# Optimization experiments

Hardware: AMD Instinct MI355X
Metric: run time of the kernel (lower is better)

## Reference

```python
import jax, jax.numpy as jnp
import numpy as np
import math

BLUR, P, SCALING = 0.05, 2.0, 0.9
DIAMETER = 8.0  # static bound on max |x-y| for unit-normal 1-D data (geomloss derives it from data)
NEG = -1e9     # masked log-weight


def _eps_schedule():
    # geomloss epsilon_schedule: diameter^p -> blur^p, geometric with ratio scaling^p
    eps = [DIAMETER ** P]
    eps += list(np.exp(np.arange(P * math.log(DIAMETER), P * math.log(BLUR), P * math.log(SCALING))))
    eps += [BLUR ** P]
    return np.asarray(eps, dtype=np.float32)


def _softmin(eps, C, h):
    # h: [m] = log-weights + dual/eps ; returns [n] = -eps*logsumexp_j(h_j - C_ij/eps)
    return -eps * jax.nn.logsumexp(h[None, :] - C / eps, axis=1)


def _sinkhorn_divergence(x, y, logw):
    # x, y: [B] 1-D point clouds for one output dim; logw: [B] masked log-weights.
    # Debiased Sinkhorn divergence S = OT_eps(a,b) - 0.5 OT(a,a) - 0.5 OT(b,b), p=2 cost |x-y|^2/2.
    Cxy = 0.5 * (x[:, None] - y[None, :]) ** 2
    Cxx = 0.5 * (x[:, None] - x[None, :]) ** 2
    Cyy = 0.5 * (y[:, None] - y[None, :]) ** 2
    eps_list = jnp.asarray(_eps_schedule())
    e0 = eps_list[0]
    f = _softmin(e0, Cxy, logw)    # dual on x for OT(a,b)
    g = _softmin(e0, Cxy.T, logw)  # dual on y for OT(a,b)
    a = _softmin(e0, Cxx, logw)    # self dual on x
    b = _softmin(e0, Cyy, logw)    # self dual on y

    def step(carry, eps):
        f, g, a, b = carry
        ft = _softmin(eps, Cxy, logw + g / eps)
        gt = _softmin(eps, Cxy.T, logw + f / eps)
        at = _softmin(eps, Cxx, logw + a / eps)
        bt = _softmin(eps, Cyy, logw + b / eps)
        return (0.5 * (f + ft), 0.5 * (g + gt), 0.5 * (a + at), 0.5 * (b + bt)), None

    (f, g, a, b), _ = jax.lax.scan(step, (f, g, a, b), eps_list)
    # last extrapolation at final eps (full updates, no damping)
    e = eps_list[-1]
    f, g = _softmin(e, Cxy, logw + g / e), _softmin(e, Cxy.T, logw + f / e)
    a = 0.5 * (a + _softmin(e, Cxx, logw + a / e))
    b = 0.5 * (b + _softmin(e, Cyy, logw + b / e))
    w = jnp.exp(logw)  # 1/n on valid samples, 0 on masked
    return jnp.sum(w * (f - a)) + jnp.sum(w * (g - b))


def reference(predictions, targets):
    # predictions, targets: [B, D]; NaNs in targets mark invalid samples per dim
    mask = ~jnp.isnan(targets)                      # [B, D]
    y = jnp.where(mask, targets, 0.0)
    counts = jnp.sum(mask, axis=0)                  # [D]
    logn = jnp.log(jnp.maximum(counts, 1).astype(predictions.dtype))
    logw = jnp.where(mask, -logn[None, :], NEG)     # [B, D]
    per_dim = jax.vmap(_sinkhorn_divergence, in_axes=(1, 1, 1))(predictions, y, logw)
    per_dim = jnp.where(counts > 1, per_dim, 0.0)   # dims with <=1 valid sample -> 0
    total = jnp.mean(per_dim)                       # weights=None -> mean over dims
    return total, per_dim


def setup_inputs() -> dict:
    key = jax.random.key(0)
    k1, k2, k3 = jax.random.split(key, 3)
    B, D = 2048, 8
    preds = jax.random.normal(k1, (B, D), dtype=jnp.float32)
    targ = jax.random.normal(k2, (B, D), dtype=jnp.float32)
    nan_mask = jax.random.uniform(k3, (B, D)) < 0.1
    targ = jnp.where(nan_mask, jnp.nan, targ)
    return {"predictions": preds, "targets": targ}
```

## Files before the change

kernel.cpp:

```cpp
#include <hip/hip_runtime.h>
#include <math.h>

#define BN 2048
#define DN 8
#define NEGW -1e9f
#define TPB 256
#define RPB 64
#define RS 16
#define JSPLIT 16
#define SLOTS (BN/2)
#define SPC (SLOTS/JSPLIT)
#define CPAD 65

typedef float f2 __attribute__((ext_vector_type(2)));

static __device__ __forceinline__ float wave_reduce_sum(float v){
  #pragma unroll
  for (int off = 32; off > 0; off >>= 1) v += __shfl_xor(v, off, 64);
  return v;
}

__global__ void setup_kernel(const float* __restrict__ pred, const float* __restrict__ targ,
                             float* __restrict__ xcol, float* __restrict__ ycol,
                             float* __restrict__ logw, float* __restrict__ counts){
  int d = blockIdx.x;
  int t = threadIdx.x;
  int lane = t & 63, wave = t >> 6;
  float mk[BN/256];
  float c = 0.f;
  for (int k = 0; k < BN/256; k++){
    int i = t + k*256;
    float tv = targ[i*DN + d];
    bool m = !(tv != tv);
    mk[k] = m ? 1.f : 0.f;
    c += mk[k];
    ycol[d*BN + i] = m ? tv : 0.f;
    xcol[d*BN + i] = pred[i*DN + d];
  }
  __shared__ float sh[4];
  __shared__ float logn_sh;
  float cw = wave_reduce_sum(c);
  if (lane == 0) sh[wave] = cw;
  __syncthreads();
  if (t == 0){
    float tot = sh[0] + sh[1] + sh[2] + sh[3];
    counts[d] = tot;
    logn_sh = logf(fmaxf(tot, 1.f));
  }
  __syncthreads();
  float ln = logn_sh;
  for (int k = 0; k < BN/256; k++){
    int i = t + k*256;
    logw[d*BN + i] = (mk[k] > 0.f) ? -ln : NEGW;
  }
}

__global__ __launch_bounds__(TPB) void sink_step(
      const float* __restrict__ xcol, const float* __restrict__ ycol,
      const float* __restrict__ logw,
      const float* __restrict__ dold, float* __restrict__ dnew,
      float eps, float inv_eps, int mode){
  const float L2E = 1.44269504088896340736f;
  const float LN2 = 0.69314718055994530942f;
  __shared__ float4 pair4[JSPLIT*CPAD];
  __shared__ float pm[JSPLIT][RPB];
  __shared__ float ps[JSPLIT][RPB];
  __shared__ float mmx[RPB];

  int bid = blockIdx.x;
  int rc  = bid & 31;
  int mat = (bid >> 5) & 3;
  int d   = bid >> 7;
  int t   = threadIdx.x;
  int rs  = t & (RS-1);
  int jc  = t >> 4;

  const float* xb = xcol + d*BN;
  const float* yb = ycol + d*BN;
  const float* lw = logw + d*BN;
  const float* ri; const float* pj; int hsel;
  switch (mat){
    case 0:  ri = xb; pj = yb; hsel = 1; break;
    case 1:  ri = yb; pj = xb; hsel = 0; break;
    case 2:  ri = xb; pj = xb; hsel = 2; break;
    default: ri = yb; pj = yb; hsel = 3; break;
  }
  const float* hd  = dold + (size_t)hsel*DN*BN + d*BN;
  const float* dmp = dold + (size_t)mat *DN*BN + d*BN;
  float*       op  = dnew + (size_t)mat *DN*BN + d*BN;

  const float c1 = L2E * inv_eps;
  const float c2 = 0.5f * inv_eps * L2E;

  const float2* pj2 = (const float2*)pj;
  const float2* lw2 = (const float2*)lw;
  const float2* hd2 = (const float2*)hd;
  #pragma unroll
  for (int k = 0; k < SLOTS/TPB; k++){
    int idx = t + k*TPB;
    int phys = idx + (idx >> 6);
    float2 y2 = pj2[idx];
    float2 l2 = lw2[idx];
    float h0 = l2.x, h1 = l2.y;
    if (mode != 0){
      float2 dd = hd2[idx];
      h0 = fmaf(dd.x, inv_eps, h0);
      h1 = fmaf(dd.y, inv_eps, h1);
    }
    pair4[phys] = make_float4(y2.x, y2.y,
                              fmaf(-c2*y2.x, y2.x, L2E*h0),
                              fmaf(-c2*y2.y, y2.y, L2E*h1));
  }

  int row0 = rc*RPB + rs;
  f2 a2[4];
  #pragma unroll
  for (int r = 0; r < 4; r++){
    float xi = ri[row0 + RS*r];
    float al = c1 * xi;
    a2[r] = (f2){al, al};
  }
  __syncthreads();

  const float4* cb = pair4 + jc*CPAD;
  f2 m2[4];
  #pragma unroll
  for (int r = 0; r < 4; r++) m2[r] = (f2){-INFINITY, -INFINITY};
  #pragma unroll 1
  for (int q = 0; q < SPC; q += 8){
    float4 P0 = cb[q+0]; float4 P1 = cb[q+1];
    float4 P2 = cb[q+2]; float4 P3 = cb[q+3];
    float4 P4 = cb[q+4]; float4 P5 = cb[q+5];
    float4 P6 = cb[q+6]; float4 P7 = cb[q+7];
    #pragma unroll
    for (int r = 0; r < 4; r++){
      f2 a = a2[r], mm = m2[r];
      mm = __builtin_elementwise_max(mm, __builtin_elementwise_fma(a, (f2){P0.x,P0.y}, (f2){P0.z,P0.w}));
      mm = __builtin_elementwise_max(mm, __builtin_elementwise_fma(a, (f2){P1.x,P1.y}, (f2){P1.z,P1.w}));
      mm = __builtin_elementwise_max(mm, __builtin_elementwise_fma(a, (f2){P2.x,P2.y}, (f2){P2.z,P2.w}));
      mm = __builtin_elementwise_max(mm, __builtin_elementwise_fma(a, (f2){P3.x,P3.y}, (f2){P3.z,P3.w}));
      mm = __builtin_elementwise_max(mm, __builtin_elementwise_fma(a, (f2){P4.x,P4.y}, (f2){P4.z,P4.w}));
      mm = __builtin_elementwise_max(mm, __builtin_elementwise_fma(a, (f2){P5.x,P5.y}, (f2){P5.z,P5.w}));
      mm = __builtin_elementwise_max(mm, __builtin_elementwise_fma(a, (f2){P6.x,P6.y}, (f2){P6.z,P6.w}));
      mm = __builtin_elementwise_max(mm, __builtin_elementwise_fma(a, (f2){P7.x,P7.y}, (f2){P7.z,P7.w}));
      m2[r] = mm;
    }
  }
  #pragma unroll
  for (int r = 0; r < 4; r++) pm[jc][rs + RS*r] = fmaxf(m2[r].x, m2[r].y);
  __syncthreads();

  if (t < RPB){
    float m = -INFINITY;
    #pragma unroll
    for (int k = 0; k < JSPLIT; k++) m = fmaxf(m, pm[k][t]);
    mmx[t] = m;
  }
  __syncthreads();

  f2 mb[4];
  #pragma unroll
  for (int r = 0; r < 4; r++){
    float m = mmx[rs + RS*r];
    mb[r] = (f2){m, m};
  }

  f2 s2[4];
  #pragma unroll
  for (int r = 0; r < 4; r++) s2[r] = (f2){0.f, 0.f};
  #pragma unroll 1
  for (int q = 0; q < SPC; q += 8){
    float4 P0 = cb[q+0]; float4 P1 = cb[q+1];
    float4 P2 = cb[q+2]; float4 P3 = cb[q+3];
    float4 P4 = cb[q+4]; float4 P5 = cb[q+5];
    float4 P6 = cb[q+6]; float4 P7 = cb[q+7];
    #pragma unroll
    for (int r = 0; r < 4; r++){
      f2 a = a2[r], m = mb[r], ss = s2[r];
      f2 v;
      v = __builtin_elementwise_fma(a, (f2){P0.x,P0.y}, (f2){P0.z,P0.w}) - m;
      ss += (f2){__builtin_amdgcn_exp2f(v.x), __builtin_amdgcn_exp2f(v.y)};
      v = __builtin_elementwise_fma(a, (f2){P1.x,P1.y}, (f2){P1.z,P1.w}) - m;
      ss += (f2){__builtin_amdgcn_exp2f(v.x), __builtin_amdgcn_exp2f(v.y)};
      v = __builtin_elementwise_fma(a, (f2){P2.x,P2.y}, (f2){P2.z,P2.w}) - m;
      ss += (f2){__builtin_amdgcn_exp2f(v.x), __builtin_amdgcn_exp2f(v.y)};
      v = __builtin_elementwise_fma(a, (f2){P3.x,P3.y}, (f2){P3.z,P3.w}) - m;
      ss += (f2){__builtin_amdgcn_exp2f(v.x), __builtin_amdgcn_exp2f(v.y)};
      v = __builtin_elementwise_fma(a, (f2){P4.x,P4.y}, (f2){P4.z,P4.w}) - m;
      ss += (f2){__builtin_amdgcn_exp2f(v.x), __builtin_amdgcn_exp2f(v.y)};
      v = __builtin_elementwise_fma(a, (f2){P5.x,P5.y}, (f2){P5.z,P5.w}) - m;
      ss += (f2){__builtin_amdgcn_exp2f(v.x), __builtin_amdgcn_exp2f(v.y)};
      v = __builtin_elementwise_fma(a, (f2){P6.x,P6.y}, (f2){P6.z,P6.w}) - m;
      ss += (f2){__builtin_amdgcn_exp2f(v.x), __builtin_amdgcn_exp2f(v.y)};
      v = __builtin_elementwise_fma(a, (f2){P7.x,P7.y}, (f2){P7.z,P7.w}) - m;
      ss += (f2){__builtin_amdgcn_exp2f(v.x), __builtin_amdgcn_exp2f(v.y)};
      s2[r] = ss;
    }
  }
  #pragma unroll
  for (int r = 0; r < 4; r++) ps[jc][rs + RS*r] = s2[r].x + s2[r].y;
  __syncthreads();

  if (t < RPB){
    int row = rc*RPB + t;
    float s = 0.f;
    #pragma unroll
    for (int k = 0; k < JSPLIT; k++) s += ps[k][t];
    float m  = mmx[t];
    float xi = ri[row];
    float beta = c2 * xi * xi;
    float lse2 = (m + __builtin_amdgcn_logf(s)) - beta;
    float tn = -eps * (LN2 * lse2);
    float outv;
    if (mode == 1 || (mode == 2 && mat >= 2)) outv = 0.5f * (dmp[row] + tn);
    else                                      outv = tn;
    op[row] = outv;
  }
}

__global__ void reduce_kernel(const float* __restrict__ dual, const float* __restrict__ logw,
                              const float* __restrict__ counts, float* __restrict__ out){
  int d = blockIdx.x;
  int t = threadIdx.x;
  int lane = t & 63, wave = t >> 6;
  float acc = 0.f;
  for (int k = 0; k < BN/256; k++){
    int i = t + k*256;
    float w  = expf(logw[d*BN + i]);
    float fv = dual[0*DN*BN + d*BN + i];
    float gv = dual[1*DN*BN + d*BN + i];
    float av = dual[2*DN*BN + d*BN + i];
    float bv = dual[3*DN*BN + d*BN + i];
    acc += w * ((fv - av) + (gv - bv));
  }
  __shared__ float sh[4];
  float aw = wave_reduce_sum(acc);
  if (lane == 0) sh[wave] = aw;
  __syncthreads();
  if (t == 0){
    float tot = sh[0] + sh[1] + sh[2] + sh[3];
    out[1 + d] = (counts[d] > 1.5f) ? tot : 0.f;
  }
}

__global__ void total_kernel(float* __restrict__ out){
  if (threadIdx.x == 0 && blockIdx.x == 0){
    float s = 0.f;
    for (int d = 0; d < DN; d++) s += out[1 + d];
    out[0] = s / (float)DN;
  }
}

extern "C" void kernel_launch(void* const* d_in, const int* in_sizes, int n_in,
                              void* d_out, int out_size, void* d_ws, size_t ws_size,
                              hipStream_t stream){
  const float* pred = (const float*)d_in[0];
  const float* targ = (const float*)d_in[1];
  float* out = (float*)d_out;
  float* ws  = (float*)d_ws;

  float* xcol   = ws;
  float* ycol   = ws + (size_t)DN*BN;
  float* logw   = ws + (size_t)2*DN*BN;
  float* counts = ws + (size_t)3*DN*BN;
  float* buf0   = ws + (size_t)3*DN*BN + 64;
  float* buf1   = buf0 + (size_t)4*DN*BN;

  float eps_list[64]; int n = 0;
  {
    const double P = 2.0, DIAM = 8.0, BLUR = 0.05, SC = 0.9;
    double ls = P*log(DIAM), le = P*log(BLUR), st = P*log(SC);
    eps_list[n++] = (float)pow(DIAM, P);
    int cnt = (int)ceil((le - ls)/st);
    for (int k = 0; k < cnt; k++) eps_list[n++] = (float)exp(ls + st*(double)k);
    eps_list[n++] = (float)(BLUR*BLUR);
  }

  setup_kernel<<<DN, 256, 0, stream>>>(pred, targ, xcol, ycol, logw, counts);

  dim3 grid(DN*4*32), blk(TPB);
  float* cur = buf0; float* nxt = buf1;
  {
    float e = eps_list[0];
    sink_step<<<grid, blk, 0, stream>>>(xcol, ycol, logw, cur, cur, e, 1.f/e, 0);
  }
  for (int k = 0; k < n; k++){
    float e = eps_list[k];
    sink_step<<<grid, blk, 0, stream>>>(xcol, ycol, logw, cur, nxt, e, 1.f/e, 1);
    float* tmp = cur; cur = nxt; nxt = tmp;
  }
  {
    float e = eps_list[n-1];
    sink_step<<<grid, blk, 0, stream>>>(xcol, ycol, logw, cur, nxt, e, 1.f/e, 2);
    float* tmp = cur; cur = nxt; nxt = tmp;
  }
  reduce_kernel<<<DN, 256, 0, stream>>>(cur, logw, counts, out);
  total_kernel<<<1, 64, 0, stream>>>(out);
}
```

Measured before the change: 1.130 ms.

## Use single-pass online logsumexp instead of separate max and sum passes

Replaces the two-pass softmin (first a max pass over shared-memory pairs, then a sum-of-exp pass) with an online logsumexp that keeps a running max and rescaled sum per row in one pass. Partial (max, sum) pairs are merged across the column splits with exp2 rescaling. This halves the shared-memory reads and FMA recomputation and drops two barriers, at the cost of one extra exp2 per 8-column block plus a few max ops. Accuracy should be equivalent, and using two accumulators keeps the dependency chains short.

```diff
diff --git a/kernel.cpp b/kernel.cpp
--- a/kernel.cpp
+++ b/kernel.cpp
@@ -63,9 +63,7 @@
   const float L2E = 1.44269504088896340736f;
   const float LN2 = 0.69314718055994530942f;
   __shared__ float4 pair4[JSPLIT*CPAD];
-  __shared__ float pm[JSPLIT][RPB];
-  __shared__ float ps[JSPLIT][RPB];
-  __shared__ float mmx[RPB];
+  __shared__ float2 pms[JSPLIT][RPB];
 
   int bid = blockIdx.x;
   int rc  = bid & 31;
@@ -123,9 +121,14 @@
   __syncthreads();
 
   const float4* cb = pair4 + jc*CPAD;
-  f2 m2[4];
-  #pragma unroll
-  for (int r = 0; r < 4; r++) m2[r] = (f2){-INFINITY, -INFINITY};
+  float mrow[4];
+  f2 sA[4], sB[4];
+  #pragma unroll
+  for (int r = 0; r < 4; r++){
+    mrow[r] = -INFINITY;
+    sA[r] = (f2){0.f, 0.f};
+    sB[r] = (f2){0.f, 0.f};
+  }
   #pragma unroll 1
   for (int q = 0; q < SPC; q += 8){
     float4 P0 = cb[q+0]; float4 P1 = cb[q+1];
@@ -134,82 +137,74 @@
     float4 P6 = cb[q+6]; float4 P7 = cb[q+7];
     #pragma unroll
     for (int r = 0; r < 4; r++){
-      f2 a = a2[r], mm = m2[r];
-      mm = __builtin_elementwise_max(mm, __builtin_elementwise_fma(a, (f2){P0.x,P0.y}, (f2){P0.z,P0.w}));
-      mm = __builtin_elementwise_max(mm, __builtin_elementwise_fma(a, (f2){P1.x,P1.y}, (f2){P1.z,P1.w}));
-      mm = __builtin_elementwise_max(mm, __builtin_elementwise_fma(a, (f2){P2.x,P2.y}, (f2){P2.z,P2.w}));
-      mm = __builtin_elementwise_max(mm, __builtin_elementwise_fma(a, (f2){P3.x,P3.y}, (f2){P3.z,P3.w}));
-      mm = __builtin_elementwise_max(mm, __builtin_elementwise_fma(a, (f2){P4.x,P4.y}, (f2){P4.z,P4.w}));
-      mm = __builtin_elementwise_max(mm, __builtin_elementwise_fma(a, (f2){P5.x,P5.y}, (f2){P5.z,P5.w}));
-      mm = __builtin_elementwise_max(mm, __builtin_elementwise_fma(a, (f2){P6.x,P6.y}, (f2){P6.z,P6.w}));
-      mm = __builtin_elementwise_max(mm, __builtin_elementwise_fma(a, (f2){P7.x,P7.y}, (f2){P7.z,P7.w}));
-      m2[r] = mm;
+      f2 a = a2[r];
+      f2 v0 = __builtin_elementwise_fma(a, (f2){P0.x,P0.y}, (f2){P0.z,P0.w});
+      f2 v1 = __builtin_elementwise_fma(a, (f2){P1.x,P1.y}, (f2){P1.z,P1.w});
+      f2 v2 = __builtin_elementwise_fma(a, (f2){P2.x,P2.y}, (f2){P2.z,P2.w});
+      f2 v3 = __builtin_elementwise_fma(a, (f2){P3.x,P3.y}, (f2){P3.z,P3.w});
+      f2 v4 = __builtin_elementwise_fma(a, (f2){P4.x,P4.y}, (f2){P4.z,P4.w});
+      f2 v5 = __builtin_elementwise_fma(a, (f2){P5.x,P5.y}, (f2){P5.z,P5.w});
+      f2 v6 = __builtin_elementwise_fma(a, (f2){P6.x,P6.y}, (f2){P6.z,P6.w});
+      f2 v7 = __builtin_elementwise_fma(a, (f2){P7.x,P7.y}, (f2){P7.z,P7.w});
+      f2 t0 = __builtin_elementwise_max(v0, v1);
+      f2 t1 = __builtin_elementwise_max(v2, v3);
+      f2 t2 = __builtin_elementwise_max(v4, v5);
+      f2 t3 = __builtin_elementwise_max(v6, v7);
+      f2 u0 = __builtin_elementwise_max(t0, t1);
+      f2 u1 = __builtin_elementwise_max(t2, t3);
+      f2 w  = __builtin_elementwise_max(u0, u1);
+      float bm = fmaxf(w.x, w.y);
+      float mo = mrow[r];
+      float mn = fmaxf(mo, bm);
+      float sc = __builtin_amdgcn_exp2f(mo - mn);
+      mrow[r] = mn;
+      f2 scv = (f2){sc, sc};
+      f2 mv  = (f2){mn, mn};
+      f2 e;
+      e = v0 - mv;
+      f2 x0 = (f2){__builtin_amdgcn_exp2f(e.x), __builtin_amdgcn_exp2f(e.y)};
+      e = v1 - mv;
+      f2 x1 = (f2){__builtin_amdgcn_exp2f(e.x), __builtin_amdgcn_exp2f(e.y)};
+      e = v2 - mv;
+      f2 x2 = (f2){__builtin_amdgcn_exp2f(e.x), __builtin_amdgcn_exp2f(e.y)};
+      e = v3 - mv;
+      f2 x3 = (f2){__builtin_amdgcn_exp2f(e.x), __builtin_amdgcn_exp2f(e.y)};
+      e = v4 - mv;
+      f2 x4 = (f2){__builtin_amdgcn_exp2f(e.x), __builtin_amdgcn_exp2f(e.y)};
+      e = v5 - mv;
+      f2 x5 = (f2){__builtin_amdgcn_exp2f(e.x), __builtin_amdgcn_exp2f(e.y)};
+      e = v6 - mv;
+      f2 x6 = (f2){__builtin_amdgcn_exp2f(e.x), __builtin_amdgcn_exp2f(e.y)};
+      e = v7 - mv;
+      f2 x7 = (f2){__builtin_amdgcn_exp2f(e.x), __builtin_amdgcn_exp2f(e.y)};
+      sA[r] = __builtin_elementwise_fma(sA[r], scv, x0);
+      sB[r] = __builtin_elementwise_fma(sB[r], scv, x1);
+      sA[r] += x2;  sB[r] += x3;
+      sA[r] += x4;  sB[r] += x5;
+      sA[r] += x6;  sB[r] += x7;
     }
   }
   #pragma unroll
-  for (int r = 0; r < 4; r++) pm[jc][rs + RS*r] = fmaxf(m2[r].x, m2[r].y);
-  __syncthreads();
-
-  if (t < RPB){
-    float m = -INFINITY;
-    #pragma unroll
-    for (int k = 0; k < JSPLIT; k++) m = fmaxf(m, pm[k][t]);
-    mmx[t] = m;
-  }
-  __syncthreads();
-
-  f2 mb[4];
-  #pragma unroll
   for (int r = 0; r < 4; r++){
-    float m = mmx[rs + RS*r];
-    mb[r] = (f2){m, m};
-  }
-
-  f2 s2[4];
-  #pragma unroll
-  for (int r = 0; r < 4; r++) s2[r] = (f2){0.f, 0.f};
-  #pragma unroll 1
-  for (int q = 0; q < SPC; q += 8){
-    float4 P0 = cb[q+0]; float4 P1 = cb[q+1];
-    float4 P2 = cb[q+2]; float4 P3 = cb[q+3];
-    float4 P4 = cb[q+4]; float4 P5 = cb[q+5];
-    float4 P6 = cb[q+6]; float4 P7 = cb[q+7];
-    #pragma unroll
-    for (int r = 0; r < 4; r++){
-      f2 a = a2[r], m = mb[r], ss = s2[r];
-      f2 v;
-      v = __builtin_elementwise_fma(a, (f2){P0.x,P0.y}, (f2){P0.z,P0.w}) - m;
-      ss += (f2){__builtin_amdgcn_exp2f(v.x), __builtin_amdgcn_exp2f(v.y)};
-      v = __builtin_elementwise_fma(a, (f2){P1.x,P1.y}, (f2){P1.z,P1.w}) - m;
-      ss += (f2){__builtin_amdgcn_exp2f(v.x), __builtin_amdgcn_exp2f(v.y)};
-      v = __builtin_elementwise_fma(a, (f2){P2.x,P2.y}, (f2){P2.z,P2.w}) - m;
-      ss += (f2){__builtin_amdgcn_exp2f(v.x), __builtin_amdgcn_exp2f(v.y)};
-      v = __builtin_elementwise_fma(a, (f2){P3.x,P3.y}, (f2){P3.z,P3.w}) - m;
-      ss += (f2){__builtin_amdgcn_exp2f(v.x), __builtin_amdgcn_exp2f(v.y)};
-      v = __builtin_elementwise_fma(a, (f2){P4.x,P4.y}, (f2){P4.z,P4.w}) - m;
-      ss += (f2){__builtin_amdgcn_exp2f(v.x), __builtin_amdgcn_exp2f(v.y)};
-      v = __builtin_elementwise_fma(a, (f2){P5.x,P5.y}, (f2){P5.z,P5.w}) - m;
-      ss += (f2){__builtin_amdgcn_exp2f(v.x), __builtin_amdgcn_exp2f(v.y)};
-      v = __builtin_elementwise_fma(a, (f2){P6.x,P6.y}, (f2){P6.z,P6.w}) - m;
-      ss += (f2){__builtin_amdgcn_exp2f(v.x), __builtin_amdgcn_exp2f(v.y)};
-      v = __builtin_elementwise_fma(a, (f2){P7.x,P7.y}, (f2){P7.z,P7.w}) - m;
-      ss += (f2){__builtin_amdgcn_exp2f(v.x), __builtin_amdgcn_exp2f(v.y)};
-      s2[r] = ss;
-    }
-  }
-  #pragma unroll
-  for (int r = 0; r < 4; r++) ps[jc][rs + RS*r] = s2[r].x + s2[r].y;
+    f2 s = sA[r] + sB[r];
+    pms[jc][rs + RS*r] = make_float2(mrow[r], s.x + s.y);
+  }
   __syncthreads();
 
   if (t < RPB){
     int row = rc*RPB + t;
+    float M = -INFINITY;
+    #pragma unroll
+    for (int k = 0; k < JSPLIT; k++) M = fmaxf(M, pms[k][t].x);
     float s = 0.f;
     #pragma unroll
-    for (int k = 0; k < JSPLIT; k++) s += ps[k][t];
-    float m  = mmx[t];
+    for (int k = 0; k < JSPLIT; k++){
+      float2 p = pms[k][t];
+      s = fmaf(p.y, __builtin_amdgcn_exp2f(p.x - M), s);
+    }
     float xi = ri[row];
     float beta = c2 * xi * xi;
-    float lse2 = (m + __builtin_amdgcn_logf(s)) - beta;
+    float lse2 = (M + __builtin_amdgcn_logf(s)) - beta;
     float tn = -eps * (LN2 * lse2);
     float outv;
     if (mode == 1 || (mode == 2 && mat >= 2)) outv = 0.5f * (dmp[row] + tn);
```

Result: faster. 1.075 ms (-4.9%).
